# Kernel tuning notes

Hardware: AMD Instinct MI355X
Metric: run time of the kernel (lower is better)

## Reference

```python
import jax, jax.numpy as jnp
import numpy as np

LUT_DIM = 33  # classic 3D color LUT grid size


def apply_lut(LUT, img):
    """Trilinear 3D-LUT apply. LUT: [3, D, D, D] (indexed [c, b, g, r]); img: [3, H, W] in ~[0,1]."""
    D = LUT.shape[1]
    x = img * (D - 1)                                   # [3, H, W] continuous grid coords
    i0 = jnp.clip(jnp.floor(x).astype(jnp.int32), 0, D - 2)
    f = x - i0.astype(x.dtype)                          # fractional offsets
    r0, g0, b0 = i0[0], i0[1], i0[2]                    # [H, W] int indices per channel
    fr, fg, fb = f[0], f[1], f[2]

    def corner(db, dg, dr):
        # 8-corner gather: [3, H, W]
        return LUT[:, b0 + db, g0 + dg, r0 + dr]

    w000 = (1 - fb) * (1 - fg) * (1 - fr)
    w001 = (1 - fb) * (1 - fg) * fr
    w010 = (1 - fb) * fg * (1 - fr)
    w011 = (1 - fb) * fg * fr
    w100 = fb * (1 - fg) * (1 - fr)
    w101 = fb * (1 - fg) * fr
    w110 = fb * fg * (1 - fr)
    w111 = fb * fg * fr

    out = (w000 * corner(0, 0, 0) + w001 * corner(0, 0, 1)
           + w010 * corner(0, 1, 0) + w011 * corner(0, 1, 1)
           + w100 * corner(1, 0, 0) + w101 * corner(1, 0, 1)
           + w110 * corner(1, 1, 0) + w111 * corner(1, 1, 1))
    return out


def setup_inputs() -> dict:
    key = jax.random.key(0)
    k1, k2, k3, k4 = jax.random.split(key, 4)
    H, W, N = 2160, 3840, 350
    gt = jax.random.uniform(k1, (3, H, W), dtype=jnp.float32)
    # Scale LUT entries by 1/N so the unweighted sum of 350 LUTs stays in ~[0,1]
    # (keeps the second apply_lut's gather indices in-range, as a real identity-ish LUT stack would).
    lut = jax.random.uniform(k2, (2, N, 3, LUT_DIM, LUT_DIM, LUT_DIM), dtype=jnp.float32) / N
    L0 = jax.random.normal(k3, (N,), dtype=jnp.float32)
    L1 = jax.random.normal(k4, (N,), dtype=jnp.float32)
    return {"gt": gt, "lut": lut, "L0": L0, "L1": L1}


def reference(gt, lut, L0, L1):
    # NOTE: the original forward computes softmax(L0)/softmax(L1) but never uses
    # the weights: it sums the LUT slices unweighted. We reproduce that faithfully;
    # the softmaxes are dead code and omitted.
    CL0 = lut[0].sum(axis=0)          # [3, D, D, D]
    I_s = apply_lut(CL0, gt)          # [3, H, W]
    CL1 = lut[1].sum(axis=0)          # [3, D, D, D]
    I_f = apply_lut(CL1, I_s)         # [3, H, W]
    return I_f
```

## Files before the change

### kernel.cpp

```cpp
#include <hip/hip_runtime.h>

#define HW_PIX (2160 * 3840)
#define D   33
#define D2  (33 * 33)
#define D3  (33 * 33 * 33)
#define M   (3 * D3)
#define NLUT 350
#define TWO_M (2 * M)

#define PIDX  (32 * 32 * 32)
#define PU4   (PIDX * 2)

__global__ __launch_bounds__(256) void reduce_kernel(
    const float* __restrict__ lut,
    float* __restrict__ accum)
{
    const int lane = threadIdx.x & 63;
    const int w    = threadIdx.x >> 6;
    const int base = blockIdx.x * 256;
    const int start = w * 87 + min(w, 2);
    const int count = 87 + (w < 2 ? 1 : 0);

    const float* srcp[4];
    bool valid[4];
    #pragma unroll
    for (int k = 0; k < 4; ++k) {
        long long u = (long long)base + lane + 64 * k;
        valid[k] = (u < TWO_M);
        long long off = valid[k]
            ? u + (u >= M ? (long long)(NLUT - 1) * M : 0LL)
            : 0LL;
        srcp[k] = lut + off + (long long)start * M;
    }

    float s0 = 0.f, s1 = 0.f, s2 = 0.f, s3 = 0.f;
    #pragma unroll 4
    for (int n = 0; n < count; ++n) {
        long long o = (long long)n * M;
        s0 += srcp[0][o];
        s1 += srcp[1][o];
        s2 += srcp[2][o];
        s3 += srcp[3][o];
    }

    __shared__ float red[4][64][4];
    red[w][lane][0] = s0;
    red[w][lane][1] = s1;
    red[w][lane][2] = s2;
    red[w][lane][3] = s3;
    __syncthreads();

    int o = threadIdx.x;
    if (base + o < TWO_M) {
        int ln = o & 63, k = o >> 6;
        float t = (red[0][ln][k] + red[1][ln][k])
                + (red[2][ln][k] + red[3][ln][k]);
        accum[base + o] = t;
    }
}

__global__ __launch_bounds__(256) void pack_kernel(
    const float* __restrict__ accum,
    uint4* __restrict__ packed)
{
    int t = blockIdx.x * 256 + threadIdx.x;
    if (t >= 2 * PIDX) return;
    int h = t >> 15;
    int e = t & (PIDX - 1);
    int b = e >> 10;
    int g = (e >> 5) & 31;
    int r = e & 31;

    const float* A = accum + (long long)h * M;
    uint4 E[2];
    #pragma unroll
    for (int bb = 0; bb < 2; ++bb) {
        unsigned q[12];
        int j = 0;
        #pragma unroll
        for (int gg = 0; gg < 2; ++gg)
            #pragma unroll
            for (int rr = 0; rr < 2; ++rr)
                #pragma unroll
                for (int c = 0; c < 3; ++c) {
                    float v = A[c * D3 + ((b + bb) * D + (g + gg)) * D + (r + rr)];
                    v = fminf(fmaxf(v, 0.0f), 1.0f);
                    q[j++] = (unsigned)(v * 1023.0f + 0.5f);
                }
        E[bb].x = q[0] | (q[1]  << 10) | (q[2]  << 20);
        E[bb].y = q[3] | (q[4]  << 10) | (q[5]  << 20);
        E[bb].z = q[6] | (q[7]  << 10) | (q[8]  << 20);
        E[bb].w = q[9] | (q[10] << 10) | (q[11] << 20);
    }
    packed[2 * t]     = E[0];
    packed[2 * t + 1] = E[1];
}

__device__ __forceinline__ void apply_q10p(const uint4* __restrict__ L,
                                           float r, float g, float b,
                                           float& outr, float& outg, float& outb)
{
    float xr = r * 32.0f, xg = g * 32.0f, xb = b * 32.0f;
    int r0 = min(max((int)floorf(xr), 0), 31);
    int g0 = min(max((int)floorf(xg), 0), 31);
    int b0 = min(max((int)floorf(xb), 0), 31);
    float fr = xr - (float)r0;
    float fg = xg - (float)g0;
    float fb = xb - (float)b0;

    int idx = (b0 << 10) + (g0 << 5) + r0;
    uint4 E0 = L[2 * idx];
    uint4 E1 = L[2 * idx + 1];

    float w00 = (1.0f - fg) * (1.0f - fr);
    float w01 = (1.0f - fg) * fr;
    float w10 = fg * (1.0f - fr);
    float w11 = fg * fr;
    float wb0 = 1.0f - fb, wb1 = fb;

    float sr, sg, sb;
    {
        float a00 = wb0 * w00, a01 = wb0 * w01, a10 = wb0 * w10, a11 = wb0 * w11;
        sr = a00 * (float)( E0.x        & 1023) + a01 * (float)( E0.y        & 1023)
           + a10 * (float)( E0.z        & 1023) + a11 * (float)( E0.w        & 1023);
        sg = a00 * (float)((E0.x >> 10) & 1023) + a01 * (float)((E0.y >> 10) & 1023)
           + a10 * (float)((E0.z >> 10) & 1023) + a11 * (float)((E0.w >> 10) & 1023);
        sb = a00 * (float)((E0.x >> 20) & 1023) + a01 * (float)((E0.y >> 20) & 1023)
           + a10 * (float)((E0.z >> 20) & 1023) + a11 * (float)((E0.w >> 20) & 1023);
    }
    {
        float a00 = wb1 * w00, a01 = wb1 * w01, a10 = wb1 * w10, a11 = wb1 * w11;
        sr += a00 * (float)( E1.x        & 1023) + a01 * (float)( E1.y        & 1023)
            + a10 * (float)( E1.z        & 1023) + a11 * (float)( E1.w        & 1023);
        sg += a00 * (float)((E1.x >> 10) & 1023) + a01 * (float)((E1.y >> 10) & 1023)
            + a10 * (float)((E1.z >> 10) & 1023) + a11 * (float)((E1.w >> 10) & 1023);
        sb += a00 * (float)((E1.x >> 20) & 1023) + a01 * (float)((E1.y >> 20) & 1023)
            + a10 * (float)((E1.z >> 20) & 1023) + a11 * (float)((E1.w >> 20) & 1023);
    }
    const float inv = 1.0f / 1023.0f;
    outr = sr * inv; outg = sg * inv; outb = sb * inv;
}

__global__ __launch_bounds__(256) void fused_apply_kernel(
    const float* __restrict__ gt,
    const uint4* __restrict__ packed,
    float* __restrict__ out)
{
    int p = blockIdx.x * 256 + threadIdx.x;
    if (p >= HW_PIX) return;

    float r = gt[p];
    float g = gt[p + HW_PIX];
    float b = gt[p + 2 * HW_PIX];

    float r1, g1, b1;
    apply_q10p(packed, r, g, b, r1, g1, b1);

    float r2, g2, b2;
    apply_q10p(packed + PU4, r1, g1, b1, r2, g2, b2);

    out[p]              = r2;
    out[p + HW_PIX]     = g2;
    out[p + 2 * HW_PIX] = b2;
}

extern "C" void kernel_launch(void* const* d_in, const int* in_sizes, int n_in,
                              void* d_out, int out_size, void* d_ws, size_t ws_size,
                              hipStream_t stream)
{
    const float* gt  = (const float*)d_in[0];
    const float* lut = (const float*)d_in[1];
    float* out = (float*)d_out;

    float* accum  = (float*)d_ws;
    uint4* packed = (uint4*)((char*)d_ws + (1 << 20));

    reduce_kernel<<<dim3((TWO_M + 255) / 256), dim3(256), 0, stream>>>(lut, accum);
    pack_kernel<<<dim3((2 * PIDX + 255) / 256), dim3(256), 0, stream>>>(accum, packed);
    fused_apply_kernel<<<dim3((HW_PIX + 255) / 256), dim3(256), 0, stream>>>(gt, packed, out);
}
```

Before: 545.8 us.

## Split LUT reduction over more blocks and process four pixels per apply thread

The LUT-stack reduction is split along the 350-LUT axis into NS slices (two when the workspace allows). This doubles the block count for the bandwidth-bound sum, and pack_kernel adds the partial sums. The apply kernel now handles four pixels per thread, using float4 nontemporal loads and stores and issuing all eight packed-LUT gathers before the interpolation math to raise memory-level parallelism. The cost is more registers per thread in the apply kernel and an extra partial-sum read in pack.

```diff
diff --git a/kernel.cpp b/kernel.cpp
--- a/kernel.cpp
+++ b/kernel.cpp
@@ -1,6 +1,7 @@
 #include <hip/hip_runtime.h>
 
 #define HW_PIX (2160 * 3840)
+#define QPIX   (HW_PIX / 4)
 #define D   33
 #define D2  (33 * 33)
 #define D3  (33 * 33 * 33)
@@ -11,36 +12,47 @@
 #define PIDX  (32 * 32 * 32)
 #define PU4   (PIDX * 2)
 
+#define HB     422
+
+typedef float        f4 __attribute__((ext_vector_type(4)));
+typedef unsigned int u4 __attribute__((ext_vector_type(4)));
+
+template<int NS>
 __global__ __launch_bounds__(256) void reduce_kernel(
     const float* __restrict__ lut,
     float* __restrict__ accum)
 {
     const int lane = threadIdx.x & 63;
     const int w    = threadIdx.x >> 6;
-    const int base = blockIdx.x * 256;
-    const int start = w * 87 + min(w, 2);
-    const int count = 87 + (w < 2 ? 1 : 0);
-
-    const float* srcp[4];
-    bool valid[4];
+    const int bid  = blockIdx.x;
+    const int s    = bid / (2 * HB);
+    const int rem  = bid - s * (2 * HB);
+    const int h    = rem / HB;
+    const int vb   = (rem - h * HB) * 256;
+
+    const int C = NLUT / NS;
+    const int q = C >> 2, r = C & 3;
+    const int start = s * C + w * q + min(w, r);
+    const int count = q + (w < r ? 1 : 0);
+
+    const float* __restrict__ hb =
+        lut + ((long long)h * NLUT + start) * M;
+
+    int off[4];
     #pragma unroll
     for (int k = 0; k < 4; ++k) {
-        long long u = (long long)base + lane + 64 * k;
-        valid[k] = (u < TWO_M);
-        long long off = valid[k]
-            ? u + (u >= M ? (long long)(NLUT - 1) * M : 0LL)
-            : 0LL;
-        srcp[k] = lut + off + (long long)start * M;
+        int v = vb + lane + 64 * k;
+        off[k] = (v < M) ? v : 0;
     }
 
     float s0 = 0.f, s1 = 0.f, s2 = 0.f, s3 = 0.f;
+    const float* p = hb;
     #pragma unroll 4
-    for (int n = 0; n < count; ++n) {
-        long long o = (long long)n * M;
-        s0 += srcp[0][o];
-        s1 += srcp[1][o];
-        s2 += srcp[2][o];
-        s3 += srcp[3][o];
+    for (int n = 0; n < count; ++n, p += M) {
+        s0 += p[off[0]];
+        s1 += p[off[1]];
+        s2 += p[off[2]];
+        s3 += p[off[3]];
     }
 
     __shared__ float red[4][64][4];
@@ -50,18 +62,20 @@
     red[w][lane][3] = s3;
     __syncthreads();
 
-    int o = threadIdx.x;
-    if (base + o < TWO_M) {
+    const int o = threadIdx.x;
+    const int v = vb + o;
+    if (v < M) {
         int ln = o & 63, k = o >> 6;
         float t = (red[0][ln][k] + red[1][ln][k])
                 + (red[2][ln][k] + red[3][ln][k]);
-        accum[base + o] = t;
+        accum[((long long)(s * 2 + h)) * M + v] = t;
     }
 }
 
 __global__ __launch_bounds__(256) void pack_kernel(
     const float* __restrict__ accum,
-    uint4* __restrict__ packed)
+    uint4* __restrict__ packed,
+    int ns)
 {
     int t = blockIdx.x * 256 + threadIdx.x;
     if (t >= 2 * PIDX) return;
@@ -83,7 +97,9 @@
             for (int rr = 0; rr < 2; ++rr)
                 #pragma unroll
                 for (int c = 0; c < 3; ++c) {
-                    float v = A[c * D3 + ((b + bb) * D + (g + gg)) * D + (r + rr)];
+                    int i = c * D3 + ((b + bb) * D + (g + gg)) * D + (r + rr);
+                    float v = A[i];
+                    for (int s = 1; s < ns; ++s) v += A[i + (long long)s * TWO_M];
                     v = fminf(fmaxf(v, 0.0f), 1.0f);
                     q[j++] = (unsigned)(v * 1023.0f + 0.5f);
                 }
@@ -96,72 +112,85 @@
     packed[2 * t + 1] = E[1];
 }
 
-__device__ __forceinline__ void apply_q10p(const uint4* __restrict__ L,
-                                           float r, float g, float b,
-                                           float& outr, float& outg, float& outb)
-{
-    float xr = r * 32.0f, xg = g * 32.0f, xb = b * 32.0f;
-    int r0 = min(max((int)floorf(xr), 0), 31);
-    int g0 = min(max((int)floorf(xg), 0), 31);
-    int b0 = min(max((int)floorf(xb), 0), 31);
-    float fr = xr - (float)r0;
-    float fg = xg - (float)g0;
-    float fb = xb - (float)b0;
-
-    int idx = (b0 << 10) + (g0 << 5) + r0;
-    uint4 E0 = L[2 * idx];
-    uint4 E1 = L[2 * idx + 1];
-
-    float w00 = (1.0f - fg) * (1.0f - fr);
-    float w01 = (1.0f - fg) * fr;
-    float w10 = fg * (1.0f - fr);
-    float w11 = fg * fr;
-    float wb0 = 1.0f - fb, wb1 = fb;
-
-    float sr, sg, sb;
-    {
-        float a00 = wb0 * w00, a01 = wb0 * w01, a10 = wb0 * w10, a11 = wb0 * w11;
-        sr = a00 * (float)( E0.x        & 1023) + a01 * (float)( E0.y        & 1023)
-           + a10 * (float)( E0.z        & 1023) + a11 * (float)( E0.w        & 1023);
-        sg = a00 * (float)((E0.x >> 10) & 1023) + a01 * (float)((E0.y >> 10) & 1023)
-           + a10 * (float)((E0.z >> 10) & 1023) + a11 * (float)((E0.w >> 10) & 1023);
-        sb = a00 * (float)((E0.x >> 20) & 1023) + a01 * (float)((E0.y >> 20) & 1023)
-           + a10 * (float)((E0.z >> 20) & 1023) + a11 * (float)((E0.w >> 20) & 1023);
-    }
-    {
-        float a00 = wb1 * w00, a01 = wb1 * w01, a10 = wb1 * w10, a11 = wb1 * w11;
-        sr += a00 * (float)( E1.x        & 1023) + a01 * (float)( E1.y        & 1023)
-            + a10 * (float)( E1.z        & 1023) + a11 * (float)( E1.w        & 1023);
-        sg += a00 * (float)((E1.x >> 10) & 1023) + a01 * (float)((E1.y >> 10) & 1023)
-            + a10 * (float)((E1.z >> 10) & 1023) + a11 * (float)((E1.w >> 10) & 1023);
-        sb += a00 * (float)((E1.x >> 20) & 1023) + a01 * (float)((E1.y >> 20) & 1023)
-            + a10 * (float)((E1.z >> 20) & 1023) + a11 * (float)((E1.w >> 20) & 1023);
+__device__ __forceinline__ void apply4(const u4* __restrict__ L,
+                                       const float* r, const float* g, const float* b,
+                                       float* pr, float* pg, float* pb)
+{
+    u4 E0[4], E1[4];
+    float fr[4], fg[4], fb[4];
+    #pragma unroll
+    for (int i = 0; i < 4; ++i) {
+        float xr = r[i] * 32.0f, xg = g[i] * 32.0f, xb = b[i] * 32.0f;
+        int r0 = min(max((int)xr, 0), 31);
+        int g0 = min(max((int)xg, 0), 31);
+        int b0 = min(max((int)xb, 0), 31);
+        fr[i] = xr - (float)r0;
+        fg[i] = xg - (float)g0;
+        fb[i] = xb - (float)b0;
+        int idx = (b0 << 10) + (g0 << 5) + r0;
+        E0[i] = L[2 * idx];
+        E1[i] = L[2 * idx + 1];
     }
     const float inv = 1.0f / 1023.0f;
-    outr = sr * inv; outg = sg * inv; outb = sb * inv;
+    #pragma unroll
+    for (int i = 0; i < 4; ++i) {
+        float w00 = (1.0f - fg[i]) * (1.0f - fr[i]);
+        float w01 = (1.0f - fg[i]) * fr[i];
+        float w10 = fg[i] * (1.0f - fr[i]);
+        float w11 = fg[i] * fr[i];
+        float wb0 = 1.0f - fb[i], wb1 = fb[i];
+
+        float sr, sg, sb;
+        {
+            float a00 = wb0 * w00, a01 = wb0 * w01, a10 = wb0 * w10, a11 = wb0 * w11;
+            sr = a00 * (float)( E0[i].x        & 1023) + a01 * (float)( E0[i].y        & 1023)
+               + a10 * (float)( E0[i].z        & 1023) + a11 * (float)( E0[i].w        & 1023);
+            sg = a00 * (float)((E0[i].x >> 10) & 1023) + a01 * (float)((E0[i].y >> 10) & 1023)
+               + a10 * (float)((E0[i].z >> 10) & 1023) + a11 * (float)((E0[i].w >> 10) & 1023);
+            sb = a00 * (float)((E0[i].x >> 20) & 1023) + a01 * (float)((E0[i].y >> 20) & 1023)
+               + a10 * (float)((E0[i].z >> 20) & 1023) + a11 * (float)((E0[i].w >> 20) & 1023);
+        }
+        {
+            float a00 = wb1 * w00, a01 = wb1 * w01, a10 = wb1 * w10, a11 = wb1 * w11;
+            sr += a00 * (float)( E1[i].x        & 1023) + a01 * (float)( E1[i].y        & 1023)
+                + a10 * (float)( E1[i].z        & 1023) + a11 * (float)( E1[i].w        & 1023);
+            sg += a00 * (float)((E1[i].x >> 10) & 1023) + a01 * (float)((E1[i].y >> 10) & 1023)
+                + a10 * (float)((E1[i].z >> 10) & 1023) + a11 * (float)((E1[i].w >> 10) & 1023);
+            sb += a00 * (float)((E1[i].x >> 20) & 1023) + a01 * (float)((E1[i].y >> 20) & 1023)
+                + a10 * (float)((E1[i].z >> 20) & 1023) + a11 * (float)((E1[i].w >> 20) & 1023);
+        }
+        pr[i] = sr * inv; pg[i] = sg * inv; pb[i] = sb * inv;
+    }
 }
 
 __global__ __launch_bounds__(256) void fused_apply_kernel(
     const float* __restrict__ gt,
-    const uint4* __restrict__ packed,
+    const u4* __restrict__ packed,
     float* __restrict__ out)
 {
-    int p = blockIdx.x * 256 + threadIdx.x;
-    if (p >= HW_PIX) return;
-
-    float r = gt[p];
-    float g = gt[p + HW_PIX];
-    float b = gt[p + 2 * HW_PIX];
-
-    float r1, g1, b1;
-    apply_q10p(packed, r, g, b, r1, g1, b1);
-
-    float r2, g2, b2;
-    apply_q10p(packed + PU4, r1, g1, b1, r2, g2, b2);
-
-    out[p]              = r2;
-    out[p + HW_PIX]     = g2;
-    out[p + 2 * HW_PIX] = b2;
+    int q = blockIdx.x * 256 + threadIdx.x;
+    if (q >= QPIX) return;
+
+    const f4* g4 = (const f4*)gt;
+    f4 Rv = __builtin_nontemporal_load(g4 + q);
+    f4 Gv = __builtin_nontemporal_load(g4 + q + QPIX);
+    f4 Bv = __builtin_nontemporal_load(g4 + q + 2 * QPIX);
+
+    float r0[4] = {Rv.x, Rv.y, Rv.z, Rv.w};
+    float g0[4] = {Gv.x, Gv.y, Gv.z, Gv.w};
+    float b0[4] = {Bv.x, Bv.y, Bv.z, Bv.w};
+    float r1[4], g1[4], b1[4], r2[4], g2[4], b2[4];
+
+    apply4(packed,       r0, g0, b0, r1, g1, b1);
+    apply4(packed + PU4, r1, g1, b1, r2, g2, b2);
+
+    f4 Ro = {r2[0], r2[1], r2[2], r2[3]};
+    f4 Go = {g2[0], g2[1], g2[2], g2[3]};
+    f4 Bo = {b2[0], b2[1], b2[2], b2[3]};
+    f4* o4 = (f4*)out;
+    __builtin_nontemporal_store(Ro, o4 + q);
+    __builtin_nontemporal_store(Go, o4 + q + QPIX);
+    __builtin_nontemporal_store(Bo, o4 + q + 2 * QPIX);
 }
 
 extern "C" void kernel_launch(void* const* d_in, const int* in_sizes, int n_in,
@@ -172,10 +201,23 @@
     const float* lut = (const float*)d_in[1];
     float* out = (float*)d_out;
 
+    const size_t packed_bytes = (size_t)2 * PIDX * 2 * sizeof(uint4);
+
+    size_t a2 = ((size_t)2 * TWO_M * sizeof(float) + 31) & ~(size_t)31;
+    size_t a1 = ((size_t)1 * TWO_M * sizeof(float) + 31) & ~(size_t)31;
+    int ns; size_t poff;
+    if (ws_size >= a2 + packed_bytes) { ns = 2; poff = a2; }
+    else                              { ns = 1; poff = a1; }
+
     float* accum  = (float*)d_ws;
-    uint4* packed = (uint4*)((char*)d_ws + (1 << 20));
-
-    reduce_kernel<<<dim3((TWO_M + 255) / 256), dim3(256), 0, stream>>>(lut, accum);
-    pack_kernel<<<dim3((2 * PIDX + 255) / 256), dim3(256), 0, stream>>>(accum, packed);
-    fused_apply_kernel<<<dim3((HW_PIX + 255) / 256), dim3(256), 0, stream>>>(gt, packed, out);
-}
+    u4*    packed = (u4*)((char*)d_ws + poff);
+
+    if (ns == 2)
+        reduce_kernel<2><<<dim3(2 * 2 * HB), dim3(256), 0, stream>>>(lut, accum);
+    else
+        reduce_kernel<1><<<dim3(1 * 2 * HB), dim3(256), 0, stream>>>(lut, accum);
+
+    pack_kernel<<<dim3((2 * PIDX + 255) / 256), dim3(256), 0, stream>>>(
+        accum, (uint4*)packed, ns);
+    fused_apply_kernel<<<dim3((QPIX + 255) / 256), dim3(256), 0, stream>>>(gt, packed, out);
+}
```

After: 555.2 us. About the same (+1.7%).
